# Performance work log

Measured on AMD Instinct MI355X. Metric: run time of the kernel, lower is better.

The kernel has to match this reference:

```python
import jax, jax.numpy as jnp
import numpy as np

MAX_DIST = 32  # unidirectional T5-style bucketing: num_buckets = 33
N_HEAD, D_K, D_V = 8, 64, 64


def setup_inputs() -> dict:
    key = jax.random.key(0)
    ks = jax.random.split(key, 9)
    B, S, D = 4, 2048, 512
    q = jax.random.normal(ks[0], (B, S, D), dtype=jnp.float32)
    k = jax.random.normal(ks[1], (B, S, D), dtype=jnp.float32)
    v = jax.random.normal(ks[2], (B, S, D), dtype=jnp.float32)
    mask = jax.random.randint(ks[3], (B, 1, 1, S), 0, 2, dtype=jnp.int32)
    sc = 1.0 / np.sqrt(D)
    Wq = jax.random.normal(ks[4], (D, D), dtype=jnp.float32) * sc
    Wk = jax.random.normal(ks[5], (D, D), dtype=jnp.float32) * sc
    Wv = jax.random.normal(ks[6], (D, D), dtype=jnp.float32) * sc
    Wfc = jax.random.normal(ks[7], (D, D), dtype=jnp.float32) * sc
    rel_bias = jax.random.normal(ks[8], (MAX_DIST + 1, N_HEAD), dtype=jnp.float32)
    return {"q": q, "k": k, "v": v, "mask": mask, "Wq": Wq, "Wk": Wk,
            "Wv": Wv, "Wfc": Wfc, "rel_bias": rel_bias}


def _rel_pos_bias(rel_bias, seq_len):
    # unidirectional: bucket = clamp(max(context - memory, 0), 0, MAX_DIST)
    pos = jnp.arange(seq_len)
    n = pos[:, None] - pos[None, :]              # context - memory = -relative_position
    bucket = jnp.clip(jnp.maximum(n, 0), 0, MAX_DIST)
    vals = rel_bias[bucket]                      # (S, S, H)
    return jnp.transpose(vals, (2, 0, 1))[None]  # (1, H, S, S)


def reference(q, k, v, mask, Wq, Wk, Wv, Wfc, rel_bias):
    B, Sq, _ = q.shape
    Sk = k.shape[1]
    scale = D_K ** (-0.5)
    qh = (q @ Wq).reshape(B, Sq, N_HEAD, D_K).transpose(0, 2, 1, 3)  # bhsd
    kh = (k @ Wk).reshape(B, Sk, N_HEAD, D_K).transpose(0, 2, 1, 3)
    vh = (v @ Wv).reshape(B, Sk, N_HEAD, D_V).transpose(0, 2, 1, 3)
    attn = jnp.einsum('bhqd,bhkd->bhqk', qh, kh) * scale
    attn = attn + _rel_pos_bias(rel_bias, Sq)
    attn = jnp.where(mask == 0, jnp.float32(-1e9), attn)
    attn = jax.nn.softmax(attn, axis=-1)          # dropout is identity at eval
    out = jnp.einsum('bhqk,bhkd->bhqd', attn, vh)
    out = out.transpose(0, 2, 1, 3).reshape(B, Sq, N_HEAD * D_V)
    out = out @ Wfc
    return out, attn
```

## Files before the change

kernel.cpp:

```cpp
#include <hip/hip_runtime.h>


typedef __attribute__((ext_vector_type(8))) short bfrag;
typedef __attribute__((ext_vector_type(4))) float f32x4;
typedef unsigned int u32;

#define MFMA16(a,b,c) __builtin_amdgcn_mfma_f32_16x16x32_bf16(a,b,c,0,0,0)

__device__ __forceinline__ void gl_lds16(const void* g, void* l){
  __builtin_amdgcn_global_load_lds((const __attribute__((address_space(1))) u32*)g,
                                   (__attribute__((address_space(3))) u32*)l, 16, 0, 0);
}
__device__ __forceinline__ short f2bs(float f){
  u32 u = __float_as_uint(f);
  u = (u + 0x7fffu + ((u>>16)&1u)) >> 16;
  return (short)u;
}
__device__ __forceinline__ float b2f(short s){
  return __uint_as_float(((u32)(unsigned short)s) << 16);
}

#define BB 4
#define HH 8
#define SS 2048
#define DD 512

#define WQT_OFF  0u
#define WKT_OFF  524288u
#define WVT_OFF  1048576u
#define WFCT_OFF 1572864u
#define QB_OFF   2097152u
#define KB_OFF   10485760u
#define VB_OFF   18874368u
#define QH_OFF   27262976u
#define KH_OFF   35651584u
#define VT_OFF   44040192u
#define OH_OFF   52428800u

__global__ __launch_bounds__(256) void conv_w_k(const float* w0,const float* w1,
                                                const float* w2,const float* w3, char* ws){
  const float* w; short* o;
  switch(blockIdx.z){
    case 0:  w=w0; o=(short*)(ws+WQT_OFF); break;
    case 1:  w=w1; o=(short*)(ws+WKT_OFF); break;
    case 2:  w=w2; o=(short*)(ws+WVT_OFF); break;
    default: w=w3; o=(short*)(ws+WFCT_OFF); break;
  }
  int t  = blockIdx.x*256 + threadIdx.x;
  int n  = t >> 6;
  int k0 = (t & 63) << 3;
  bfrag v;
  #pragma unroll
  for (int j=0;j<8;++j) v[j] = f2bs(w[(k0+j)*512 + n]);
  *(bfrag*)(o + n*512 + k0) = v;
}

__global__ __launch_bounds__(256) void conv_x_k(const float* x0,const float* x1,
                                                const float* x2, char* ws){
  const float* x; short* o;
  switch(blockIdx.z){
    case 0:  x=x0; o=(short*)(ws+QB_OFF); break;
    case 1:  x=x1; o=(short*)(ws+KB_OFF); break;
    default: x=x2; o=(short*)(ws+VB_OFF); break;
  }
  int i = (blockIdx.x*256 + threadIdx.x) << 3;
  float4 a = *(const float4*)(x+i);
  float4 b = *(const float4*)(x+i+4);
  bfrag v;
  v[0]=f2bs(a.x); v[1]=f2bs(a.y); v[2]=f2bs(a.z); v[3]=f2bs(a.w);
  v[4]=f2bs(b.x); v[5]=f2bs(b.y); v[6]=f2bs(b.z); v[7]=f2bs(b.w);
  *(bfrag*)(o+i) = v;
}

__device__ void gemm_core(const short* A, const short* Bt, char* Cout, int mode, int bid){
  __shared__ __align__(16) char lds[32768];
  int i0, j0;
  if (mode==1){ i0 = (bid&3)<<7; j0 = (bid>>2)<<7; }
  else        { i0 = (bid>>2)<<7; j0 = (bid&3)<<7; }
  int tid = threadIdx.x;
  int l = tid & 63, w = tid >> 6;
  int wr = (w>>1)<<6, wc = (w&1)<<6;
  int l15 = l & 15, l4 = l >> 4;
  f32x4 acc[4][4];
  #pragma unroll
  for(int a=0;a<4;++a)
    #pragma unroll
    for(int b=0;b<4;++b) acc[a][b] = (f32x4){0.f,0.f,0.f,0.f};
  const char* Ab = (const char*)A;
  const char* Bb = (const char*)Bt;
  for (int kk=0; kk<8; ++kk){
    #pragma unroll
    for (int it=0; it<4; ++it){
      int ci = it*256 + tid;
      int row = ci>>3, cc = ci&7;
      gl_lds16(Ab + (size_t)(i0+row)*1024 + kk*128 + ((cc^(row&7))<<4),
               lds + ((it*256 + w*64)<<4));
      gl_lds16(Bb + (size_t)(j0+row)*1024 + kk*128 + ((cc^(row&7))<<4),
               lds + 16384 + ((it*256 + w*64)<<4));
    }
    asm volatile("s_waitcnt vmcnt(0)" ::: "memory");
    __syncthreads();
    #pragma unroll
    for (int kb=0; kb<2; ++kb){
      bfrag af[4], bf[4];
      #pragma unroll
      for (int mi=0;mi<4;++mi){
        int row = wr + mi*16 + l15;
        af[mi] = *(const bfrag*)(lds + row*128 + (((kb*4 + l4) ^ (row&7))<<4));
      }
      #pragma unroll
      for (int ni=0;ni<4;++ni){
        int row = wc + ni*16 + l15;
        bf[ni] = *(const bfrag*)(lds + 16384 + row*128 + (((kb*4 + l4) ^ (row&7))<<4));
      }
      #pragma unroll
      for (int mi=0;mi<4;++mi)
        #pragma unroll
        for (int ni=0;ni<4;++ni)
          acc[mi][ni] = MFMA16(af[mi], bf[ni], acc[mi][ni]);
    }
    __syncthreads();
  }
  #pragma unroll
  for (int mi=0;mi<4;++mi){
    #pragma unroll
    for (int ni=0;ni<4;++ni){
      #pragma unroll
      for (int r=0;r<4;++r){
        int i = i0 + wr + mi*16 + (l4<<2) + r;
        int j = j0 + wc + ni*16 + l15;
        float v = acc[mi][ni][r];
        if (mode==2){
          ((float*)Cout)[(size_t)i*512 + j] = v;
        } else if (mode==0){
          size_t o = ((size_t)(((i>>11)<<3) + (j>>6))*2048 + (size_t)(i&2047))*64 + (j&63);
          ((short*)Cout)[o] = f2bs(v);
        } else {
          size_t o = ((size_t)(((j>>11)<<3) + (i>>6))*64 + (size_t)(i&63))*2048 + (j&2047);
          ((short*)Cout)[o] = f2bs(v);
        }
      }
    }
  }
}

__global__ __launch_bounds__(256,2) void gemm_proj_k(char* ws){
  switch(blockIdx.z){
    case 0:  gemm_core((const short*)(ws+QB_OFF),  (const short*)(ws+WQT_OFF), ws+QH_OFF, 0, blockIdx.x); break;
    case 1:  gemm_core((const short*)(ws+KB_OFF),  (const short*)(ws+WKT_OFF), ws+KH_OFF, 0, blockIdx.x); break;
    default: gemm_core((const short*)(ws+WVT_OFF), (const short*)(ws+VB_OFF),  ws+VT_OFF, 1, blockIdx.x); break;
  }
}
__global__ __launch_bounds__(256,2) void gemm_final_k(char* ws, float* out){
  gemm_core((const short*)(ws+OH_OFF), (const short*)(ws+WFCT_OFF), (char*)out, 2, blockIdx.x);
}

#define KV_OFF_L    131072
#define MSK_OFF_L   147456
#define BIAS_OFF_L  155648
#define WSUM_OFF_L  155808
#define RECIP_OFF_L 156320
#define LDS_TOTAL   156448

__global__ __launch_bounds__(512,1) void attn_k(char* ws, const int* mask,
                                                const float* rel_bias, float* attn_out){
  extern __shared__ __align__(16) char sm[];
  int tid = threadIdx.x;
  int l = tid & 63, w = tid >> 6;
  int l15 = l & 15, l4 = l >> 4;
  int wq = w >> 2, wk = w & 3;
  int qblk = blockIdx.x, bh = blockIdx.y;
  int b = bh >> 3, h = bh & 7;
  const short* qhb = (const short*)(ws+QH_OFF) + (size_t)bh*SS*64;
  const char*  khb = ws + KH_OFF + (size_t)bh*SS*128;
  const char*  vtb = ws + VT_OFF + (size_t)bh*64*SS*2;

  {
    const int4* m4 = (const int4*)(mask + b*SS);
    int4 ma = m4[tid];
    float4* mf = (float4*)(sm + MSK_OFF_L);
    mf[tid] = make_float4(ma.x?1.f:0.f, ma.y?1.f:0.f, ma.z?1.f:0.f, ma.w?1.f:0.f);
  }
  if (tid < 33) ((float*)(sm+BIAS_OFF_L))[tid] = rel_bias[tid*HH + h];

  int wrow  = wq << 4;
  int qrow0 = (qblk<<5) + wrow;
  bfrag qf0 = *(const bfrag*)(qhb + (size_t)(qrow0 + l15)*64 + l4*8);
  bfrag qf1 = *(const bfrag*)(qhb + (size_t)(qrow0 + l15)*64 + 32 + l4*8);
  float rsum[4] = {0.f,0.f,0.f,0.f};
  char* kv0 = sm + KV_OFF_L;
  char* kv1 = sm + KV_OFF_L + 8192;
  const float* biasl = (const float*)(sm+BIAS_OFF_L);
  const float* maskl = (const float*)(sm+MSK_OFF_L);

  auto stageK = [&](int kc){
    const char* kt = khb + (size_t)kc*8192;
    char* dst = (kc&1)?kv1:kv0;
    int row = tid>>3, cc = tid&7;
    gl_lds16(kt + row*128 + ((cc^(row&7))<<4), dst + (tid<<4));
  };
  auto stageV = [&](int vc){
    char* dst = (vc&1)?kv1:kv0;
    int row = tid>>3, cc = tid&7;
    gl_lds16(vtb + (size_t)row*4096 + (vc<<7) + ((cc^(row&7))<<4),
             dst + (tid<<4));
  };

  stageK(0); stageK(1);
  __syncthreads();

  for (int kc=0; kc<32; ++kc){
    if (kc<31) { asm volatile("s_waitcnt vmcnt(1)" ::: "memory"); }
    else       { asm volatile("s_waitcnt vmcnt(0)" ::: "memory"); }
    __builtin_amdgcn_s_barrier();
    const char* kb = (kc&1)?kv1:kv0;
    int rowk = (wk<<4) + l15;
    bfrag b0 = *(const bfrag*)(kb + rowk*128 + (((l4  )^(rowk&7))<<4));
    bfrag b1 = *(const bfrag*)(kb + rowk*128 + (((4+l4)^(rowk&7))<<4));
    f32x4 acc = (f32x4){0.f,0.f,0.f,0.f};
    acc = MFMA16(qf0, b0, acc);
    acc = MFMA16(qf1, b1, acc);
    int kpos = (kc<<6) + rowk;
    float mval = maskl[kpos];
    int rl0 = wrow + (l4<<2);
    int qg0 = (qblk<<5) + rl0;
    #pragma unroll
    for (int r=0;r<4;++r){
      int n = qg0 + r - kpos;
      n = n<0 ? 0 : (n>32 ? 32 : n);
      float s = acc[r]*0.125f + biasl[n];
      float p = mval * __expf(s);
      rsum[r] += p;
      int rowl = rl0 + r;
      int byte = kpos<<1;
      int ch = (byte>>4) ^ (rowl&15);
      *(short*)(sm + rowl*4096 + (ch<<4) + (byte&15)) = f2bs(p);
    }
    __builtin_amdgcn_s_barrier();
    if (kc+2<32) stageK(kc+2);
  }

  stageV(0); stageV(1);

  {
    float* wsum = (float*)(sm+WSUM_OFF_L);
    #pragma unroll
    for (int r=0;r<4;++r){
      float s = rsum[r];
      s += __shfl_xor(s,1); s += __shfl_xor(s,2);
      s += __shfl_xor(s,4); s += __shfl_xor(s,8);
      if (l15==0) wsum[w*16 + (l4<<2) + r] = s;
    }
  }
  __syncthreads();
  if (tid < 32){
    float* wsum = (float*)(sm+WSUM_OFF_L);
    int iq = tid >> 4, i = tid & 15;
    float t = wsum[(iq*4+0)*16 + i] + wsum[(iq*4+1)*16 + i]
            + wsum[(iq*4+2)*16 + i] + wsum[(iq*4+3)*16 + i];
    ((float*)(sm+RECIP_OFF_L))[tid] = 1.f/t;
  }
  __syncthreads();
  const float* recip = (const float*)(sm+RECIP_OFF_L);

  f32x4 acco = (f32x4){0.f,0.f,0.f,0.f};
  int dbase = wk << 4;
  int prow = wrow + l15;
  for (int vc=0; vc<32; ++vc){
    if (vc<31) { asm volatile("s_waitcnt vmcnt(1)" ::: "memory"); }
    else       { asm volatile("s_waitcnt vmcnt(0)" ::: "memory"); }
    __builtin_amdgcn_s_barrier();
    const char* vb = (vc&1)?kv1:kv0;
    #pragma unroll
    for (int m=0;m<2;++m){
      int pcol = (vc<<6) + (m<<5) + (l4<<3);
      int pch = (pcol>>3) ^ (prow&15);
      bfrag af = *(const bfrag*)(sm + prow*4096 + (pch<<4));
      int drow = dbase + l15;
      bfrag bv = *(const bfrag*)(vb + drow*128 + ((((m<<2)+l4)^(drow&7))<<4));
      acco = MFMA16(af, bv, acco);
    }
    __builtin_amdgcn_s_barrier();
    if (vc+2<32) stageV(vc+2);
  }

  {
    short* oh = (short*)(ws + OH_OFF);
    #pragma unroll
    for (int r=0;r<4;++r){
      int rowl = wrow + (l4<<2) + r;
      float rc = recip[rowl];
      size_t sg = (size_t)b*SS + (qblk<<5) + rowl;
      oh[sg*512 + h*64 + dbase + l15] = f2bs(acco[r]*rc);
    }
  }

  {
    float* dst0 = attn_out + (size_t)bh*SS*SS + (size_t)(qblk<<5)*SS;
    #pragma unroll
    for (int rr=0; rr<4; ++rr){
      int rowl = (w<<2) + rr;
      float rc = recip[rowl];
      float* dst = dst0 + (size_t)rowl*SS;
      #pragma unroll
      for (int it=0; it<4; ++it){
        int col = it*512 + (l<<3);
        int ch = (col>>3) ^ (rowl&15);
        bfrag pv = *(const bfrag*)(sm + rowl*4096 + (ch<<4));
        f32x4 o0 = (f32x4){b2f(pv[0])*rc, b2f(pv[1])*rc, b2f(pv[2])*rc, b2f(pv[3])*rc};
        f32x4 o1 = (f32x4){b2f(pv[4])*rc, b2f(pv[5])*rc, b2f(pv[6])*rc, b2f(pv[7])*rc};
        __builtin_nontemporal_store(o0, (f32x4*)(dst+col));
        __builtin_nontemporal_store(o1, (f32x4*)(dst+col+4));
      }
    }
  }
}

extern "C" void kernel_launch(void* const* d_in, const int* in_sizes, int n_in,
                              void* d_out, int out_size, void* d_ws, size_t ws_size,
                              hipStream_t stream){
  const float* q   = (const float*)d_in[0];
  const float* k   = (const float*)d_in[1];
  const float* v   = (const float*)d_in[2];
  const int*  mask = (const int*)  d_in[3];
  const float* Wq  = (const float*)d_in[4];
  const float* Wk  = (const float*)d_in[5];
  const float* Wv  = (const float*)d_in[6];
  const float* Wfc = (const float*)d_in[7];
  const float* rb  = (const float*)d_in[8];
  char* ws = (char*)d_ws;
  float* out  = (float*)d_out;
  float* attn = out + (size_t)BB*SS*512;

  (void)hipFuncSetAttribute((const void*)attn_k,
        hipFuncAttributeMaxDynamicSharedMemorySize, LDS_TOTAL);

  conv_w_k<<<dim3(128,1,4), 256, 0, stream>>>(Wq, Wk, Wv, Wfc, ws);
  conv_x_k<<<dim3(2048,1,3), 256, 0, stream>>>(q, k, v, ws);
  gemm_proj_k<<<dim3(256,1,3), 256, 0, stream>>>(ws);
  attn_k<<<dim3(64,32), 512, LDS_TOTAL, stream>>>(ws, mask, rb, attn);
  gemm_final_k<<<dim3(256,1,1), 256, 0, stream>>>(ws, out);
}
```

Baseline: 366.3 us.

## Drop LDS K/V staging, load fragments directly from global and reorder grid

The attention kernel stops double-buffering K and V chunks through LDS with barriers each step. Each wave now reads its own K rows and V columns straight from global memory into registers, and handles 256 key positions across both 16-row query halves. This removes the per-chunk barrier synchronisation. The grid is transposed so blocks sharing a query block but different heads launch adjacently, which may improve L2 reuse. The cost is uncoalesced, unpipelined global loads whose latency is hidden only by unrolling, with no sharing of K/V across waves through LDS.

```diff
diff --git a/kernel.cpp b/kernel.cpp
--- a/kernel.cpp
+++ b/kernel.cpp
@@ -155,12 +155,11 @@
   gemm_core((const short*)(ws+OH_OFF), (const short*)(ws+WFCT_OFF), (char*)out, 2, blockIdx.x);
 }
 
-#define KV_OFF_L    131072
-#define MSK_OFF_L   147456
-#define BIAS_OFF_L  155648
-#define WSUM_OFF_L  155808
-#define RECIP_OFF_L 156320
-#define LDS_TOTAL   156448
+#define MSK_OFF_L   131072
+#define BIAS_OFF_L  139264
+#define WSUM_OFF_L  139424
+#define RECIP_OFF_L 140448
+#define LDS_TOTAL   140576
 
 __global__ __launch_bounds__(512,1) void attn_k(char* ws, const int* mask,
                                                 const float* rel_bias, float* attn_out){
@@ -168,8 +167,7 @@
   int tid = threadIdx.x;
   int l = tid & 63, w = tid >> 6;
   int l15 = l & 15, l4 = l >> 4;
-  int wq = w >> 2, wk = w & 3;
-  int qblk = blockIdx.x, bh = blockIdx.y;
+  int bh = blockIdx.x, qblk = blockIdx.y;
   int b = bh >> 3, h = bh & 7;
   const short* qhb = (const short*)(ws+QH_OFF) + (size_t)bh*SS*64;
   const char*  khb = ws + KH_OFF + (size_t)bh*SS*128;
@@ -183,112 +181,92 @@
   }
   if (tid < 33) ((float*)(sm+BIAS_OFF_L))[tid] = rel_bias[tid*HH + h];
 
-  int wrow  = wq << 4;
-  int qrow0 = (qblk<<5) + wrow;
-  bfrag qf0 = *(const bfrag*)(qhb + (size_t)(qrow0 + l15)*64 + l4*8);
-  bfrag qf1 = *(const bfrag*)(qhb + (size_t)(qrow0 + l15)*64 + 32 + l4*8);
-  float rsum[4] = {0.f,0.f,0.f,0.f};
-  char* kv0 = sm + KV_OFF_L;
-  char* kv1 = sm + KV_OFF_L + 8192;
+  int qrow = (qblk<<5) + l15;
+  bfrag qA0 = *(const bfrag*)(qhb + (size_t)qrow*64 + l4*8);
+  bfrag qA1 = *(const bfrag*)(qhb + (size_t)qrow*64 + 32 + l4*8);
+  bfrag qB0 = *(const bfrag*)(qhb + (size_t)(qrow+16)*64 + l4*8);
+  bfrag qB1 = *(const bfrag*)(qhb + (size_t)(qrow+16)*64 + 32 + l4*8);
   const float* biasl = (const float*)(sm+BIAS_OFF_L);
   const float* maskl = (const float*)(sm+MSK_OFF_L);
-
-  auto stageK = [&](int kc){
-    const char* kt = khb + (size_t)kc*8192;
-    char* dst = (kc&1)?kv1:kv0;
-    int row = tid>>3, cc = tid&7;
-    gl_lds16(kt + row*128 + ((cc^(row&7))<<4), dst + (tid<<4));
-  };
-  auto stageV = [&](int vc){
-    char* dst = (vc&1)?kv1:kv0;
-    int row = tid>>3, cc = tid&7;
-    gl_lds16(vtb + (size_t)row*4096 + (vc<<7) + ((cc^(row&7))<<4),
-             dst + (tid<<4));
-  };
-
-  stageK(0); stageK(1);
+  float rsum[8] = {0.f,0.f,0.f,0.f,0.f,0.f,0.f,0.f};
+
   __syncthreads();
 
-  for (int kc=0; kc<32; ++kc){
-    if (kc<31) { asm volatile("s_waitcnt vmcnt(1)" ::: "memory"); }
-    else       { asm volatile("s_waitcnt vmcnt(0)" ::: "memory"); }
-    __builtin_amdgcn_s_barrier();
-    const char* kb = (kc&1)?kv1:kv0;
-    int rowk = (wk<<4) + l15;
-    bfrag b0 = *(const bfrag*)(kb + rowk*128 + (((l4  )^(rowk&7))<<4));
-    bfrag b1 = *(const bfrag*)(kb + rowk*128 + (((4+l4)^(rowk&7))<<4));
-    f32x4 acc = (f32x4){0.f,0.f,0.f,0.f};
-    acc = MFMA16(qf0, b0, acc);
-    acc = MFMA16(qf1, b1, acc);
-    int kpos = (kc<<6) + rowk;
-    float mval = maskl[kpos];
-    int rl0 = wrow + (l4<<2);
-    int qg0 = (qblk<<5) + rl0;
-    #pragma unroll
-    for (int r=0;r<4;++r){
-      int n = qg0 + r - kpos;
-      n = n<0 ? 0 : (n>32 ? 32 : n);
-      float s = acc[r]*0.125f + biasl[n];
-      float p = mval * __expf(s);
-      rsum[r] += p;
-      int rowl = rl0 + r;
-      int byte = kpos<<1;
-      int ch = (byte>>4) ^ (rowl&15);
-      *(short*)(sm + rowl*4096 + (ch<<4) + (byte&15)) = f2bs(p);
-    }
-    __builtin_amdgcn_s_barrier();
-    if (kc+2<32) stageK(kc+2);
-  }
-
-  stageV(0); stageV(1);
+  int wbase = w << 8;
+  #pragma unroll 2
+  for (int t=0; t<16; ++t){
+    int rowk = wbase + (t<<4) + l15;
+    const char* kr = khb + (size_t)rowk*128 + (l4<<4);
+    bfrag b0 = *(const bfrag*)(kr);
+    bfrag b1 = *(const bfrag*)(kr + 64);
+    f32x4 acc0 = (f32x4){0.f,0.f,0.f,0.f};
+    f32x4 acc1 = (f32x4){0.f,0.f,0.f,0.f};
+    acc0 = MFMA16(qA0, b0, acc0);
+    acc0 = MFMA16(qA1, b1, acc0);
+    acc1 = MFMA16(qB0, b0, acc1);
+    acc1 = MFMA16(qB1, b1, acc1);
+    float mval = maskl[rowk];
+    int rl0 = l4<<2;
+    int byte = rowk<<1;
+    #pragma unroll
+    for (int hf=0; hf<2; ++hf){
+      f32x4 acc = hf ? acc1 : acc0;
+      #pragma unroll
+      for (int r=0;r<4;++r){
+        int rowl = (hf<<4) + rl0 + r;
+        int n = (qblk<<5) + rowl - rowk;
+        n = n<0 ? 0 : (n>32 ? 32 : n);
+        float s = acc[r]*0.125f + biasl[n];
+        float p = mval * __expf(s);
+        rsum[(hf<<2)+r] += p;
+        int ch = (byte>>4) ^ (rowl&15);
+        *(short*)(sm + rowl*4096 + (ch<<4) + (byte&15)) = f2bs(p);
+      }
+    }
+  }
 
   {
     float* wsum = (float*)(sm+WSUM_OFF_L);
     #pragma unroll
-    for (int r=0;r<4;++r){
-      float s = rsum[r];
+    for (int i=0;i<8;++i){
+      float s = rsum[i];
       s += __shfl_xor(s,1); s += __shfl_xor(s,2);
       s += __shfl_xor(s,4); s += __shfl_xor(s,8);
-      if (l15==0) wsum[w*16 + (l4<<2) + r] = s;
+      if (l15==0){
+        int rowl = ((i>>2)<<4) + (l4<<2) + (i&3);
+        wsum[(w<<5) + rowl] = s;
+      }
     }
   }
   __syncthreads();
   if (tid < 32){
     float* wsum = (float*)(sm+WSUM_OFF_L);
-    int iq = tid >> 4, i = tid & 15;
-    float t = wsum[(iq*4+0)*16 + i] + wsum[(iq*4+1)*16 + i]
-            + wsum[(iq*4+2)*16 + i] + wsum[(iq*4+3)*16 + i];
+    float t = 0.f;
+    #pragma unroll
+    for (int i=0;i<8;++i) t += wsum[(i<<5) + tid];
     ((float*)(sm+RECIP_OFF_L))[tid] = 1.f/t;
   }
   __syncthreads();
   const float* recip = (const float*)(sm+RECIP_OFF_L);
 
   f32x4 acco = (f32x4){0.f,0.f,0.f,0.f};
-  int dbase = wk << 4;
-  int prow = wrow + l15;
-  for (int vc=0; vc<32; ++vc){
-    if (vc<31) { asm volatile("s_waitcnt vmcnt(1)" ::: "memory"); }
-    else       { asm volatile("s_waitcnt vmcnt(0)" ::: "memory"); }
-    __builtin_amdgcn_s_barrier();
-    const char* vb = (vc&1)?kv1:kv0;
-    #pragma unroll
-    for (int m=0;m<2;++m){
-      int pcol = (vc<<6) + (m<<5) + (l4<<3);
-      int pch = (pcol>>3) ^ (prow&15);
-      bfrag af = *(const bfrag*)(sm + prow*4096 + (pch<<4));
-      int drow = dbase + l15;
-      bfrag bv = *(const bfrag*)(vb + drow*128 + ((((m<<2)+l4)^(drow&7))<<4));
-      acco = MFMA16(af, bv, acco);
-    }
-    __builtin_amdgcn_s_barrier();
-    if (vc+2<32) stageV(vc+2);
+  int wq = w >> 2, dbase = (w&3)<<4;
+  int prow = (wq<<4) + l15;
+  int drow = dbase + l15;
+  const char* vr = vtb + (size_t)drow*4096 + (l4<<4);
+  #pragma unroll 4
+  for (int vc=0; vc<64; ++vc){
+    int ch = ((vc<<2) + l4) ^ l15;
+    bfrag af = *(const bfrag*)(sm + prow*4096 + (ch<<4));
+    bfrag bv = *(const bfrag*)(vr + (vc<<6));
+    acco = MFMA16(af, bv, acco);
   }
 
   {
     short* oh = (short*)(ws + OH_OFF);
     #pragma unroll
     for (int r=0;r<4;++r){
-      int rowl = wrow + (l4<<2) + r;
+      int rowl = (wq<<4) + (l4<<2) + r;
       float rc = recip[rowl];
       size_t sg = (size_t)b*SS + (qblk<<5) + rowl;
       oh[sg*512 + h*64 + dbase + l15] = f2bs(acco[r]*rc);
@@ -338,6 +316,6 @@
   conv_w_k<<<dim3(128,1,4), 256, 0, stream>>>(Wq, Wk, Wv, Wfc, ws);
   conv_x_k<<<dim3(2048,1,3), 256, 0, stream>>>(q, k, v, ws);
   gemm_proj_k<<<dim3(256,1,3), 256, 0, stream>>>(ws);
-  attn_k<<<dim3(64,32), 512, LDS_TOTAL, stream>>>(ws, mask, rb, attn);
+  attn_k<<<dim3(32,64), 512, LDS_TOTAL, stream>>>(ws, mask, rb, attn);
   gemm_final_k<<<dim3(256,1,1), 256, 0, stream>>>(ws, out);
 }
```

New measurement: 397.5 us. 1.09x slower.
